# Kernel optimization log

Measured on AMD Instinct MI355X. Metric: run time of the kernel, lower is better.

Reference implementation:

```python
import jax, jax.numpy as jnp
import numpy as np

N_NODES = 50000
N_EDGES = 1600000
DIM = 128
HEADS = 8
HEAD_DIM = DIM // HEADS


def setup_inputs() -> dict:
    key = jax.random.key(0)
    ks = jax.random.split(key, 12)
    s = 1.0 / np.sqrt(DIM)
    return {
        "x": jax.random.normal(ks[0], (N_NODES, DIM), dtype=jnp.float32),
        "src": jax.random.randint(ks[1], (N_EDGES,), 0, N_NODES, dtype=jnp.int32),
        "dst": jax.random.randint(ks[2], (N_EDGES,), 0, N_NODES, dtype=jnp.int32),
        "Wq": jax.random.uniform(ks[3], (DIM, DIM), jnp.float32, -s, s),
        "bq": jax.random.uniform(ks[4], (DIM,), jnp.float32, -s, s),
        "Wk": jax.random.uniform(ks[5], (DIM, DIM), jnp.float32, -s, s),
        "bk": jax.random.uniform(ks[6], (DIM,), jnp.float32, -s, s),
        "Wv": jax.random.uniform(ks[7], (DIM, DIM), jnp.float32, -s, s),
        "bv": jax.random.uniform(ks[8], (DIM,), jnp.float32, -s, s),
        "Wo": jax.random.uniform(ks[9], (DIM, DIM), jnp.float32, -s, s),
        "bo": jax.random.uniform(ks[10], (DIM,), jnp.float32, -s, s),
    }


def reference(x, src, dst, Wq, bq, Wk, bk, Wv, bv, Wo, bo):
    # Linear projections (torch Linear: x @ W.T + b), split into heads
    q = (x @ Wq.T + bq).reshape(-1, HEADS, HEAD_DIM)  # [N, H, Dh]
    k = (x @ Wk.T + bk).reshape(-1, HEADS, HEAD_DIM)
    v = (x @ Wv.T + bv).reshape(-1, HEADS, HEAD_DIM)

    # u_dot_v: per-edge dot of q[src] and k[dst] per head -> [E, H]
    scores = jnp.einsum("ehd,ehd->eh", q[src], k[dst]) / np.sqrt(HEAD_DIM).astype(np.float32)

    # edge_softmax: softmax over edges grouped by destination node
    m = jax.ops.segment_max(scores, dst, num_segments=N_NODES)  # [N, H]
    e = jnp.exp(scores - m[dst])
    z = jax.ops.segment_sum(e, dst, num_segments=N_NODES)  # [N, H]
    probs = e / z[dst]  # [E, H]

    # u_mul_e_sum: scatter-add of v[src] * probs into dst -> [N, H, Dh]
    msg = v[src] * probs[:, :, None]
    agg = jax.ops.segment_sum(msg, dst, num_segments=N_NODES)

    out = agg.reshape(-1, DIM) @ Wo.T + bo  # dropout p=0.0 -> identity
    return out
```

## Files before the change

### kernel.cpp

```cpp
#include <hip/hip_runtime.h>
#include <hip/hip_bf16.h>
#include <math.h>

#define N_NODES 50000
#define N_EDGES 1600000
#define NBUCK 256
#define NBUCK_ACTIVE ((N_NODES + 255) / 256)
#define P1_BLOCKS ((N_EDGES + 4095) / 4096)
#define CAP 9216
#define QKV_BLOCKS ((N_NODES + 63) / 64)

typedef short bf16x8 __attribute__((ext_vector_type(8)));
typedef float f32x4 __attribute__((ext_vector_type(4)));

#define SC2 0.3606737602222409f
#define MNEG -1.0e30f

static __device__ __forceinline__ unsigned short f2bf(float f) {
  unsigned int b = __float_as_uint(f);
  unsigned int r = (b + 0x7FFFu + ((b >> 16) & 1u)) >> 16;
  return (unsigned short)r;
}
static __device__ __forceinline__ float bf_lo(unsigned int u) {
  return __uint_as_float(u << 16);
}
static __device__ __forceinline__ float bf_hi(unsigned int u) {
  return __uint_as_float(u & 0xFFFF0000u);
}

__global__ __launch_bounds__(256) void bucket_partition(
    const int* __restrict__ src, const int* __restrict__ dst,
    int* __restrict__ bcursor, unsigned int* __restrict__ packed,
    const float* __restrict__ Wq, const float* __restrict__ Wk,
    const float* __restrict__ Wv, const float* __restrict__ Wo,
    unsigned short* __restrict__ wb) {
  const int t = threadIdx.x;
  if (blockIdx.x < 64) {
    int idx = blockIdx.x * 256 + t;
    wb[idx] = f2bf(Wq[idx]);
    wb[16384 + idx] = f2bf(Wk[idx]);
    wb[32768 + idx] = f2bf(Wv[idx]);
    wb[49152 + idx] = f2bf(Wo[idx]);
  }

  __shared__ int h[NBUCK];
  __shared__ int sd[NBUCK];
  __shared__ int lofs[NBUCK];
  __shared__ int gbase[NBUCK];
  __shared__ unsigned int stage[4096];
  __shared__ unsigned short sbin[4096];

  h[t] = 0;
  __syncthreads();
  const int ebase = blockIdx.x * 4096;
  const int count = min(4096, N_EDGES - ebase);
  const int base4 = blockIdx.x * 1024;
  unsigned int val[16];
  int binrank[16];
#pragma unroll
  for (int i = 0; i < 4; ++i) {
    int i4 = base4 + i * 256 + t;
    if (i4 < N_EDGES / 4) {
      int4 s4 = ((const int4*)src)[i4];
      int4 d4 = ((const int4*)dst)[i4];
      int ss[4] = {s4.x, s4.y, s4.z, s4.w};
      int dd[4] = {d4.x, d4.y, d4.z, d4.w};
#pragma unroll
      for (int j = 0; j < 4; ++j) {
        val[i * 4 + j] = ((unsigned)dd[j] << 16) | (unsigned)ss[j];
        int bin = dd[j] >> 8;
        int r = atomicAdd(&h[bin], 1);
        binrank[i * 4 + j] = (bin << 16) | r;
      }
    } else {
#pragma unroll
      for (int j = 0; j < 4; ++j) binrank[i * 4 + j] = -1;
    }
  }
  __syncthreads();
  const int own = h[t];
  if (own > 0) gbase[t] = atomicAdd(&bcursor[t], own);
  sd[t] = own;
  __syncthreads();
  for (int d = 1; d < NBUCK; d <<= 1) {
    int v = (t >= d) ? sd[t - d] : 0;
    __syncthreads();
    sd[t] += v;
    __syncthreads();
  }
  lofs[t] = sd[t] - own;
  __syncthreads();
#pragma unroll
  for (int i = 0; i < 16; ++i) {
    if (binrank[i] >= 0) {
      int bin = binrank[i] >> 16;
      int r = binrank[i] & 0xFFFF;
      int slot = lofs[bin] + r;
      stage[slot] = val[i];
      sbin[slot] = (unsigned short)bin;
    }
  }
  __syncthreads();
  for (int j = t; j < count; j += 256) {
    int b = sbin[j];
    packed[(size_t)b * CAP + gbase[b] + (j - lofs[b])] = stage[j];
  }
}

__global__ __launch_bounds__(256) void qkv_and_finalize(
    const float* __restrict__ x, const unsigned short* __restrict__ wb,
    const float* __restrict__ bq, const float* __restrict__ bk,
    const float* __restrict__ bv,
    unsigned short* __restrict__ qrec, unsigned short* __restrict__ kb,
    unsigned short* __restrict__ vrec,
    const unsigned int* __restrict__ packed, const int* __restrict__ bcursor,
    int* __restrict__ ebeg, int* __restrict__ eend,
    unsigned short* __restrict__ ssrc, int nrows) {
  __shared__ __align__(16) unsigned short sbuf[64 * 136];
  const int tid = threadIdx.x;

  if (blockIdx.x < QKV_BLOCKS) {
    const int w = tid >> 6;
    const int lane = tid & 63;
    const int lr = lane & 15;
    const int kg = lane >> 4;
    const int rowbase = blockIdx.x * 64;
    const int arow = min(rowbase + w * 16 + lr, nrows - 1);

    bf16x8 af[4];
    const float* xr = x + (size_t)arow * 128;
#pragma unroll
    for (int ksub = 0; ksub < 4; ++ksub) {
      const int k0 = ksub * 32 + kg * 8;
      float4 f0 = *(const float4*)(xr + k0);
      float4 f1 = *(const float4*)(xr + k0 + 4);
      af[ksub][0] = (short)f2bf(f0.x);
      af[ksub][1] = (short)f2bf(f0.y);
      af[ksub][2] = (short)f2bf(f0.z);
      af[ksub][3] = (short)f2bf(f0.w);
      af[ksub][4] = (short)f2bf(f1.x);
      af[ksub][5] = (short)f2bf(f1.y);
      af[ksub][6] = (short)f2bf(f1.z);
      af[ksub][7] = (short)f2bf(f1.w);
    }

    for (int p = 0; p < 3; ++p) {
      const unsigned short* wp = wb + p * 16384;
      const float* bias = (p == 0) ? bq : (p == 1) ? bk : bv;
      unsigned short* gout = (p == 0) ? qrec : (p == 1) ? kb : vrec;
      f32x4 acc[8];
#pragma unroll
      for (int nt = 0; nt < 8; ++nt) {
        float b = bias[nt * 16 + lr];
        acc[nt] = (f32x4){b, b, b, b};
      }
#pragma unroll
      for (int ksub = 0; ksub < 4; ++ksub) {
#pragma unroll
        for (int nt = 0; nt < 8; ++nt) {
          bf16x8 bfr = *(const bf16x8*)(wp + (size_t)(nt * 16 + lr) * 128 +
                                        ksub * 32 + kg * 8);
          acc[nt] = __builtin_amdgcn_mfma_f32_16x16x32_bf16(af[ksub], bfr,
                                                            acc[nt], 0, 0, 0);
        }
      }
      __syncthreads();
#pragma unroll
      for (int nt = 0; nt < 8; ++nt) {
        int col = nt * 16 + lr;
#pragma unroll
        for (int r = 0; r < 4; ++r)
          sbuf[(w * 16 + kg * 4 + r) * 136 + col] = f2bf(acc[nt][r]);
      }
      __syncthreads();
#pragma unroll
      for (int i = 0; i < 4; ++i) {
        int idx = i * 256 + tid;
        int lrow = idx >> 4;
        int u16o = (idx & 15) * 8;
        int grow = rowbase + lrow;
        if (grow < nrows)
          *(uint4*)(gout + (size_t)grow * 128 + u16o) =
              *(const uint4*)&sbuf[lrow * 136 + u16o];
      }
    }
  } else {
    int* cnt = (int*)sbuf;
    int* sd = cnt + NBUCK;
    int* cur = sd + NBUCK;
    const int t = tid;
    const int b = blockIdx.x - QKV_BLOCKS;
    const int beg = b * CAP;
    const int n_in_bucket = min(bcursor[b], CAP);
    cnt[t] = 0;
    __syncthreads();
    for (int e = t; e < n_in_bucket; e += 256)
      atomicAdd(&cnt[(packed[beg + e] >> 16) & 255], 1);
    __syncthreads();
    const int own = cnt[t];
    sd[t] = own;
    __syncthreads();
    for (int d = 1; d < NBUCK; d <<= 1) {
      int v = (t >= d) ? sd[t - d] : 0;
      __syncthreads();
      sd[t] += v;
      __syncthreads();
    }
    const int excl = sd[t] - own;
    cur[t] = excl;
    const int node = b * 256 + t;
    if (node < N_NODES) {
      ebeg[node] = beg + excl;
      eend[node] = beg + excl + own;
    }
    __syncthreads();
    for (int e = t; e < n_in_bucket; e += 256) {
      unsigned int p = packed[beg + e];
      int local = (p >> 16) & 255;
      int r = atomicAdd(&cur[local], 1);
      ssrc[beg + r] = (unsigned short)(p & 0xFFFFu);
    }
  }
}

__global__ __launch_bounds__(1024, 4) void edge_agg_out(
    const unsigned short* __restrict__ qrec, const unsigned short* __restrict__ vrec,
    const unsigned short* __restrict__ kb,
    const int* __restrict__ ebeg, const int* __restrict__ eend,
    const unsigned short* __restrict__ ssrc,
    const unsigned short* __restrict__ wo, const float* __restrict__ bo,
    float* __restrict__ out) {
  __shared__ __align__(16) unsigned short aggs[16 * 136];
  const int wid = threadIdx.x >> 6;
  const int lane = threadIdx.x & 63;
  const int l16 = lane & 15;
  const int qq = lane >> 4;
  const int loff = l16 * 8;
  const int nbase = blockIdx.x * 16;
  const int n = nbase + wid;

#define DOT8(t0)                                                       \
  (bf_lo(t0.x) * k0 + bf_hi(t0.x) * k1 + bf_lo(t0.y) * k2 +            \
   bf_hi(t0.y) * k3 + bf_lo(t0.z) * k4 + bf_hi(t0.z) * k5 +            \
   bf_lo(t0.w) * k6 + bf_hi(t0.w) * k7)

#define ACC8(pe, tv)                        \
  a0 = fmaf(pe, bf_lo(tv.x), a0);           \
  a1 = fmaf(pe, bf_hi(tv.x), a1);           \
  a2 = fmaf(pe, bf_lo(tv.y), a2);           \
  a3 = fmaf(pe, bf_hi(tv.y), a3);           \
  a4 = fmaf(pe, bf_lo(tv.z), a4);           \
  a5 = fmaf(pe, bf_hi(tv.z), a5);           \
  a6 = fmaf(pe, bf_lo(tv.w), a6);           \
  a7 = fmaf(pe, bf_hi(tv.w), a7)

  {
    const uint4 ku = *(const uint4*)(kb + (size_t)n * 128 + loff);
    const float k0 = bf_lo(ku.x), k1 = bf_hi(ku.x);
    const float k2 = bf_lo(ku.y), k3 = bf_hi(ku.y);
    const float k4 = bf_lo(ku.z), k5 = bf_hi(ku.z);
    const float k6 = bf_lo(ku.w), k7 = bf_hi(ku.w);

    const int start = ebeg[n];
    const int end = eend[n];

    float zz = 0.0f;
    float a0 = 0, a1 = 0, a2 = 0, a3 = 0, a4 = 0, a5 = 0, a6 = 0, a7 = 0;

    int base = start;
    for (; base + 16 <= end; base += 16) {
      int sA = ssrc[base + qq];
      int sB = ssrc[base + 4 + qq];
      int sC = ssrc[base + 8 + qq];
      int sD = ssrc[base + 12 + qq];
      const uint4 qA = *(const uint4*)(qrec + ((size_t)sA << 7) + loff);
      const uint4 vA = *(const uint4*)(vrec + ((size_t)sA << 7) + loff);
      const uint4 qB = *(const uint4*)(qrec + ((size_t)sB << 7) + loff);
      const uint4 vB = *(const uint4*)(vrec + ((size_t)sB << 7) + loff);
      const uint4 qC = *(const uint4*)(qrec + ((size_t)sC << 7) + loff);
      const uint4 vC = *(const uint4*)(vrec + ((size_t)sC << 7) + loff);
      const uint4 qD = *(const uint4*)(qrec + ((size_t)sD << 7) + loff);
      const uint4 vD = *(const uint4*)(vrec + ((size_t)sD << 7) + loff);

      float pA = DOT8(qA);
      float pB = DOT8(qB);
      float pC = DOT8(qC);
      float pD = DOT8(qD);
      pA += __shfl_xor(pA, 1);
      pB += __shfl_xor(pB, 1);
      pC += __shfl_xor(pC, 1);
      pD += __shfl_xor(pD, 1);
      float peA = __builtin_amdgcn_exp2f(pA * SC2);
      float peB = __builtin_amdgcn_exp2f(pB * SC2);
      float peC = __builtin_amdgcn_exp2f(pC * SC2);
      float peD = __builtin_amdgcn_exp2f(pD * SC2);
      zz += (peA + peB) + (peC + peD);
      ACC8(peA, vA);
      ACC8(peB, vB);
      ACC8(peC, vC);
      ACC8(peD, vD);
    }
    for (; base < end; base += 4) {
      int idx = base + qq;
      bool valid = idx < end;
      int s = ssrc[valid ? idx : end - 1];
      const uint4 q0 = *(const uint4*)(qrec + ((size_t)s << 7) + loff);
      const uint4 v0 = *(const uint4*)(vrec + ((size_t)s << 7) + loff);
      float p = DOT8(q0);
      p += __shfl_xor(p, 1);
      float pe = __builtin_amdgcn_exp2f(valid ? p * SC2 : MNEG);
      zz += pe;
      ACC8(pe, v0);
    }

#pragma unroll
    for (int off = 16; off <= 32; off <<= 1) {
      zz += __shfl_xor(zz, off);
      a0 += __shfl_xor(a0, off);
      a1 += __shfl_xor(a1, off);
      a2 += __shfl_xor(a2, off);
      a3 += __shfl_xor(a3, off);
      a4 += __shfl_xor(a4, off);
      a5 += __shfl_xor(a5, off);
      a6 += __shfl_xor(a6, off);
      a7 += __shfl_xor(a7, off);
    }
    float inv = (zz > 0.0f) ? 1.0f / zz : 0.0f;

    if (qq == 0) {
      unsigned short o[8] = {f2bf(a0 * inv), f2bf(a1 * inv), f2bf(a2 * inv),
                             f2bf(a3 * inv), f2bf(a4 * inv), f2bf(a5 * inv),
                             f2bf(a6 * inv), f2bf(a7 * inv)};
      *(uint4*)&aggs[wid * 136 + loff] = *(const uint4*)o;
    }
  }
#undef DOT8
#undef ACC8

  __syncthreads();

  if (wid < 8) {
    bf16x8 af[4];
#pragma unroll
    for (int ksub = 0; ksub < 4; ++ksub)
      af[ksub] = *(const bf16x8*)&aggs[l16 * 136 + ksub * 32 + qq * 8];

    float b = bo[wid * 16 + l16];
    f32x4 acc = (f32x4){b, b, b, b};
#pragma unroll
    for (int ksub = 0; ksub < 4; ++ksub) {
      bf16x8 bfr = *(const bf16x8*)(wo + (size_t)(wid * 16 + l16) * 128 +
                                    ksub * 32 + qq * 8);
      acc = __builtin_amdgcn_mfma_f32_16x16x32_bf16(af[ksub], bfr, acc, 0, 0, 0);
    }
    int col = wid * 16 + l16;
#pragma unroll
    for (int r = 0; r < 4; ++r) {
      int grow = nbase + qq * 4 + r;
      out[(size_t)grow * 128 + col] = acc[r];
    }
  }
}

extern "C" void kernel_launch(void* const* d_in, const int* in_sizes, int n_in,
                              void* d_out, int out_size, void* d_ws, size_t ws_size,
                              hipStream_t stream) {
  const float* x  = (const float*)d_in[0];
  const int* src  = (const int*)d_in[1];
  const int* dst  = (const int*)d_in[2];
  const float* Wq = (const float*)d_in[3];
  const float* bq = (const float*)d_in[4];
  const float* Wk = (const float*)d_in[5];
  const float* bk = (const float*)d_in[6];
  const float* Wv = (const float*)d_in[7];
  const float* bv = (const float*)d_in[8];
  const float* Wo = (const float*)d_in[9];
  const float* bo = (const float*)d_in[10];
  float* out = (float*)d_out;

  char* ws = (char*)d_ws;
  size_t off = 0;
  auto carve = [&](size_t bytes) {
    size_t r = off;
    off = (off + bytes + 255) & ~(size_t)255;
    return r;
  };
  unsigned short* qrec = (unsigned short*)(ws + carve((size_t)N_NODES * 256));
  unsigned short* vrec = (unsigned short*)(ws + carve((size_t)N_NODES * 256));
  unsigned short* kb   = (unsigned short*)(ws + carve((size_t)N_NODES * 256));
  unsigned int* packed = (unsigned int*)(ws + carve((size_t)NBUCK * CAP * 4));
  unsigned short* ssrc = (unsigned short*)(ws + carve((size_t)NBUCK * CAP * 2));
  int* ebeg    = (int*)(ws + carve((size_t)N_NODES * sizeof(int)));
  int* eend    = (int*)(ws + carve((size_t)N_NODES * sizeof(int)));
  int* bcursor = (int*)(ws + carve(NBUCK * sizeof(int)));
  unsigned short* wb = (unsigned short*)(ws + carve((size_t)4 * 128 * 128 * 2));

  hipMemsetAsync(bcursor, 0, NBUCK * sizeof(int), stream);

  bucket_partition<<<P1_BLOCKS, 256, 0, stream>>>(src, dst, bcursor, packed,
                                                  Wq, Wk, Wv, Wo, wb);

  qkv_and_finalize<<<QKV_BLOCKS + NBUCK_ACTIVE, 256, 0, stream>>>(
      x, wb, bq, bk, bv, qrec, kb, vrec, packed, bcursor, ebeg, eend, ssrc,
      N_NODES);

  edge_agg_out<<<N_NODES / 16, 1024, 0, stream>>>(qrec, vrec, kb, ebeg, eend,
                                                  ssrc, wb + 3 * 16384, bo, out);
}
```

Measured before the change: 203.1 us.

## Compute output projection per-wave via shuffles, dropping LDS staging and block sync

```diff
diff --git a/kernel.cpp b/kernel.cpp
--- a/kernel.cpp
+++ b/kernel.cpp
@@ -223,21 +223,19 @@
   }
 }
 
-__global__ __launch_bounds__(1024, 4) void edge_agg_out(
+__global__ __launch_bounds__(256, 4) void edge_agg_out(
     const unsigned short* __restrict__ qrec, const unsigned short* __restrict__ vrec,
     const unsigned short* __restrict__ kb,
     const int* __restrict__ ebeg, const int* __restrict__ eend,
     const unsigned short* __restrict__ ssrc,
     const unsigned short* __restrict__ wo, const float* __restrict__ bo,
     float* __restrict__ out) {
-  __shared__ __align__(16) unsigned short aggs[16 * 136];
   const int wid = threadIdx.x >> 6;
   const int lane = threadIdx.x & 63;
   const int l16 = lane & 15;
   const int qq = lane >> 4;
   const int loff = l16 * 8;
-  const int nbase = blockIdx.x * 16;
-  const int n = nbase + wid;
+  const int n = blockIdx.x * 4 + wid;
 
 #define DOT8(t0)                                                       \
   (bf_lo(t0.x) * k0 + bf_hi(t0.x) * k1 + bf_lo(t0.y) * k2 +            \
@@ -254,6 +252,8 @@
   a6 = fmaf(pe, bf_lo(tv.w), a6);           \
   a7 = fmaf(pe, bf_hi(tv.w), a7)
 
+  float zz = 0.0f;
+  float a0 = 0, a1 = 0, a2 = 0, a3 = 0, a4 = 0, a5 = 0, a6 = 0, a7 = 0;
   {
     const uint4 ku = *(const uint4*)(kb + (size_t)n * 128 + loff);
     const float k0 = bf_lo(ku.x), k1 = bf_hi(ku.x);
@@ -263,9 +263,6 @@
 
     const int start = ebeg[n];
     const int end = eend[n];
-
-    float zz = 0.0f;
-    float a0 = 0, a1 = 0, a2 = 0, a3 = 0, a4 = 0, a5 = 0, a6 = 0, a7 = 0;
 
     int base = start;
     for (; base + 16 <= end; base += 16) {
@@ -312,53 +309,55 @@
       zz += pe;
       ACC8(pe, v0);
     }
-
-#pragma unroll
-    for (int off = 16; off <= 32; off <<= 1) {
-      zz += __shfl_xor(zz, off);
-      a0 += __shfl_xor(a0, off);
-      a1 += __shfl_xor(a1, off);
-      a2 += __shfl_xor(a2, off);
-      a3 += __shfl_xor(a3, off);
-      a4 += __shfl_xor(a4, off);
-      a5 += __shfl_xor(a5, off);
-      a6 += __shfl_xor(a6, off);
-      a7 += __shfl_xor(a7, off);
-    }
-    float inv = (zz > 0.0f) ? 1.0f / zz : 0.0f;
-
-    if (qq == 0) {
-      unsigned short o[8] = {f2bf(a0 * inv), f2bf(a1 * inv), f2bf(a2 * inv),
-                             f2bf(a3 * inv), f2bf(a4 * inv), f2bf(a5 * inv),
-                             f2bf(a6 * inv), f2bf(a7 * inv)};
-      *(uint4*)&aggs[wid * 136 + loff] = *(const uint4*)o;
-    }
   }
 #undef DOT8
 #undef ACC8
 
-  __syncthreads();
-
-  if (wid < 8) {
-    bf16x8 af[4];
-#pragma unroll
-    for (int ksub = 0; ksub < 4; ++ksub)
-      af[ksub] = *(const bf16x8*)&aggs[l16 * 136 + ksub * 32 + qq * 8];
-
-    float b = bo[wid * 16 + l16];
-    f32x4 acc = (f32x4){b, b, b, b};
-#pragma unroll
-    for (int ksub = 0; ksub < 4; ++ksub) {
-      bf16x8 bfr = *(const bf16x8*)(wo + (size_t)(wid * 16 + l16) * 128 +
+#pragma unroll
+  for (int off = 16; off <= 32; off <<= 1) {
+    zz += __shfl_xor(zz, off);
+    a0 += __shfl_xor(a0, off);
+    a1 += __shfl_xor(a1, off);
+    a2 += __shfl_xor(a2, off);
+    a3 += __shfl_xor(a3, off);
+    a4 += __shfl_xor(a4, off);
+    a5 += __shfl_xor(a5, off);
+    a6 += __shfl_xor(a6, off);
+    a7 += __shfl_xor(a7, off);
+  }
+  float inv = (zz > 0.0f) ? 1.0f / zz : 0.0f;
+
+  unsigned int pk0 = (unsigned)f2bf(a0 * inv) | ((unsigned)f2bf(a1 * inv) << 16);
+  unsigned int pk1 = (unsigned)f2bf(a2 * inv) | ((unsigned)f2bf(a3 * inv) << 16);
+  unsigned int pk2 = (unsigned)f2bf(a4 * inv) | ((unsigned)f2bf(a5 * inv) << 16);
+  unsigned int pk3 = (unsigned)f2bf(a6 * inv) | ((unsigned)f2bf(a7 * inv) << 16);
+
+  f32x4 acc[8];
+#pragma unroll
+  for (int nt = 0; nt < 8; ++nt) {
+    float b = bo[nt * 16 + l16];
+    acc[nt] = (f32x4){b, b, b, b};
+  }
+#pragma unroll
+  for (int ksub = 0; ksub < 4; ++ksub) {
+    int srcl = ksub * 4 + qq;
+    int4 aw;
+    aw.x = __shfl((int)pk0, srcl);
+    aw.y = __shfl((int)pk1, srcl);
+    aw.z = __shfl((int)pk2, srcl);
+    aw.w = __shfl((int)pk3, srcl);
+    bf16x8 af = *(bf16x8*)&aw;
+#pragma unroll
+    for (int nt = 0; nt < 8; ++nt) {
+      bf16x8 bfr = *(const bf16x8*)(wo + (size_t)(nt * 16 + l16) * 128 +
                                     ksub * 32 + qq * 8);
-      acc = __builtin_amdgcn_mfma_f32_16x16x32_bf16(af[ksub], bfr, acc, 0, 0, 0);
-    }
-    int col = wid * 16 + l16;
-#pragma unroll
-    for (int r = 0; r < 4; ++r) {
-      int grow = nbase + qq * 4 + r;
-      out[(size_t)grow * 128 + col] = acc[r];
-    }
+      acc[nt] = __builtin_amdgcn_mfma_f32_16x16x32_bf16(af, bfr, acc[nt], 0, 0, 0);
+    }
+  }
+  if (lane < 16) {
+#pragma unroll
+    for (int nt = 0; nt < 8; ++nt)
+      out[(size_t)n * 128 + nt * 16 + l16] = acc[nt][0];
   }
 }
 
@@ -404,6 +403,6 @@
       x, wb, bq, bk, bv, qrec, kb, vrec, packed, bcursor, ebeg, eend, ssrc,
       N_NODES);
 
-  edge_agg_out<<<N_NODES / 16, 1024, 0, stream>>>(qrec, vrec, kb, ebeg, eend,
-                                                  ssrc, wb + 3 * 16384, bo, out);
-}
+  edge_agg_out<<<N_NODES / 4, 256, 0, stream>>>(qrec, vrec, kb, ebeg, eend,
+                                                ssrc, wb + 3 * 16384, bo, out);
+}
```

Result: slower. 294.6 us (+45.1%).
